# Optimization experiments

Hardware: AMD Instinct MI355X
Metric: run time of the kernel (lower is better)

The kernel has to match this reference:

```python
import jax, jax.numpy as jnp
import numpy as np


def setup_inputs() -> dict:
    key = jax.random.key(0)
    k1, k2, k3 = jax.random.split(key, 3)
    B, C, H, W = 16, 256, 48, 48
    INTER = C // 2
    x = jax.random.normal(k1, (B, C, H, W), dtype=jnp.float32)
    # nn.init.normal_(weight, std=0.01); 1x1 conv kernels stored as (out, in)
    theta_w = 0.01 * jax.random.normal(k2, (INTER, C), dtype=jnp.float32)
    phi_w = 0.01 * jax.random.normal(k3, (INTER, C), dtype=jnp.float32)
    theta_b = jnp.zeros((INTER,), dtype=jnp.float32)
    phi_b = jnp.zeros((INTER,), dtype=jnp.float32)
    return {"x": x, "theta_w": theta_w, "theta_b": theta_b, "phi_w": phi_w, "phi_b": phi_b}


def reference(x, theta_w, theta_b, phi_w, phi_b):
    b, c, h, w = x.shape
    inter = theta_w.shape[0]
    n = h * w
    # 1x1 conv == channel-wise linear projection
    theta_x = jnp.einsum('bchw,kc->bkhw', x, theta_w) + theta_b[None, :, None, None]
    phi_x = jnp.einsum('bchw,kc->bkhw', x, phi_w) + phi_b[None, :, None, None]
    q = theta_x.reshape(b, inter, n)   # [b, k, n]
    kmat = phi_x.reshape(b, inter, n)  # [b, k, n]
    g = x.reshape(b, c, n)             # [b, c, n]
    # f = theta^T @ phi : [b, n, n], scaled then softmaxed over last dim
    f = jnp.einsum('bkn,bkm->bnm', q, kmat) / jnp.sqrt(jnp.asarray(inter, x.dtype))
    f = jax.nn.softmax(f, axis=-1)
    # y = f @ g^T : [b, c, n]
    y = jnp.einsum('bnm,bcm->bcn', f, g)
    return y.reshape(b, c, h, w)
```

## Files before the change

### kernel.cpp

```cpp
#include <hip/hip_runtime.h>
#include <hip/hip_bf16.h>

#define B_SZ 16
#define C_IN 256
#define N_SP 2304
#define K_INT 128
#define NTILE 36
#define MT 32
#define MITER 72

typedef __attribute__((ext_vector_type(8))) short short8;
typedef __attribute__((ext_vector_type(4))) float f32x4;

__device__ inline unsigned pk_bf16(float a, float b) {
  float2 f; f.x = a; f.y = b;
  __hip_bfloat162 h = __float22bfloat162_rn(f);
  unsigned u;
  __builtin_memcpy(&u, &h, sizeof(u));
  return u;
}

__global__ __launch_bounds__(256) void proj_kernel(
    const float* __restrict__ x,
    const float* __restrict__ theta_w, const float* __restrict__ theta_b,
    const float* __restrict__ phi_w,   const float* __restrict__ phi_b,
    short* __restrict__ Qt, short* __restrict__ Kt, short* __restrict__ Gbf)
{
  __shared__ short Xl[64][264];

  const int b  = blockIdx.x / NTILE;
  const int n0 = (blockIdx.x % NTILE) * 64;
  const int t  = threadIdx.x;

  {
    const float* xrow = x + ((size_t)b * C_IN + t) * N_SP + n0;
    unsigned tp[32];
#pragma unroll
    for (int i = 0; i < 16; ++i) {
      float4 v = ((const float4*)xrow)[i];
      tp[2*i]   = pk_bf16(v.x, v.y);
      tp[2*i+1] = pk_bf16(v.z, v.w);
    }
    uint4* grow = (uint4*)(Gbf + ((size_t)b * C_IN + t) * N_SP + n0);
#pragma unroll
    for (int i = 0; i < 8; ++i) {
      uint4 u; u.x = tp[4*i]; u.y = tp[4*i+1]; u.z = tp[4*i+2]; u.w = tp[4*i+3];
      grow[i] = u;
    }
#pragma unroll
    for (int j = 0; j < 32; ++j) {
      Xl[2*j][t]   = (short)tp[j];
      Xl[2*j+1][t] = (short)(tp[j] >> 16);
    }
  }
  __syncthreads();

  const int wave = t >> 6, lane = t & 63;
  const int col = lane & 15, quad = lane >> 4;

  f32x4 acc[2][2][4];
#pragma unroll
  for (int p = 0; p < 2; ++p)
#pragma unroll
    for (int kr = 0; kr < 2; ++kr)
#pragma unroll
      for (int j = 0; j < 4; ++j) {
        acc[p][kr][j][0] = 0.f; acc[p][kr][j][1] = 0.f;
        acc[p][kr][j][2] = 0.f; acc[p][kr][j][3] = 0.f;
      }

#pragma unroll
  for (int cs = 0; cs < 8; ++cs) {
    const int c0 = cs * 32;
    short8 afr[2][2];
#pragma unroll
    for (int p = 0; p < 2; ++p) {
      const float* W = p ? phi_w : theta_w;
#pragma unroll
      for (int kr = 0; kr < 2; ++kr) {
        const int k = wave * 32 + kr * 16 + col;
        const float* wp = W + (size_t)k * C_IN + c0 + quad * 8;
        float4 w0 = ((const float4*)wp)[0];
        float4 w1 = ((const float4*)wp)[1];
        unsigned u[4];
        u[0] = pk_bf16(w0.x, w0.y); u[1] = pk_bf16(w0.z, w0.w);
        u[2] = pk_bf16(w1.x, w1.y); u[3] = pk_bf16(w1.z, w1.w);
        short8 a;
        __builtin_memcpy(&a, u, sizeof(a));
        afr[p][kr] = a;
      }
    }
#pragma unroll
    for (int j = 0; j < 4; ++j) {
      short8 bfr = *(const short8*)&Xl[j * 16 + col][c0 + quad * 8];
#pragma unroll
      for (int p = 0; p < 2; ++p)
#pragma unroll
        for (int kr = 0; kr < 2; ++kr)
          acc[p][kr][j] = __builtin_amdgcn_mfma_f32_16x16x32_bf16(
              afr[p][kr], bfr, acc[p][kr][j], 0, 0, 0);
    }
  }

#pragma unroll
  for (int p = 0; p < 2; ++p) {
    const float* bias = p ? phi_b : theta_b;
    short* dst = p ? Kt : Qt;
#pragma unroll
    for (int kr = 0; kr < 2; ++kr) {
      const int k0 = wave * 32 + kr * 16 + quad * 4;
      float4 bv = *(const float4*)(bias + k0);
#pragma unroll
      for (int j = 0; j < 4; ++j) {
        const int n = n0 + j * 16 + col;
        f32x4 v = acc[p][kr][j];
        uint2 sv;
        sv.x = pk_bf16(v[0] + bv.x, v[1] + bv.y);
        sv.y = pk_bf16(v[2] + bv.z, v[3] + bv.w);
        *(uint2*)(dst + ((size_t)b * N_SP + n) * K_INT + k0) = sv;
      }
    }
  }
}

__global__ __launch_bounds__(256) void attn_kernel(
    const short* __restrict__ Qt, const short* __restrict__ Kt,
    const short* __restrict__ Gbf, float* __restrict__ out)
{
  __shared__ __align__(16) char smem[49152];

  const int b   = blockIdx.x / NTILE;
  const int qn0 = (blockIdx.x % NTILE) * 64;
  const int t = threadIdx.x;
  const int wave = t >> 6, lane = t & 63;
  const int col = lane & 15, quad = lane >> 4;

  const short* Ktb = Kt  + (size_t)b * N_SP * K_INT;
  const short* Gb  = Gbf + (size_t)b * C_IN * N_SP;

  short8 qf[4];
  {
    const short* qb = Qt + ((size_t)b * N_SP + qn0 + wave * 16 + col) * K_INT + quad * 8;
#pragma unroll
    for (int kk = 0; kk < 4; ++kk) qf[kk] = *(const short8*)(qb + kk * 32);
  }

  f32x4 yacc[16];
#pragma unroll
  for (int i = 0; i < 16; ++i) {
    yacc[i][0] = 0.f; yacc[i][1] = 0.f; yacc[i][2] = 0.f; yacc[i][3] = 0.f;
  }
  f32x4 lacc;
  lacc[0] = 0.f; lacc[1] = 0.f; lacc[2] = 0.f; lacc[3] = 0.f;

  short8 ones;
#pragma unroll
  for (int j = 0; j < 8; ++j) ones[j] = (short)0x3F80;

  const float SC2 = 0.12754859f;

  const int KW = (t >> 4) * 256 + ((((t & 15) ^ ((t >> 4) & 7))) << 4);
  const int GW = 8192 + (t >> 2) * 64 + ((((t & 3) ^ ((t >> 3) & 3))) << 4);
  int KR[4];
#pragma unroll
  for (int kk = 0; kk < 4; ++kk)
    KR[kk] = col * 256 + ((((kk << 2) + quad) ^ (col & 7)) << 4);
  const int GR = 8192 + col * 64 + ((quad ^ ((col >> 1) & 3)) << 4);

  const int koff = (t >> 4) * K_INT + (t & 15) * 8;
  const int goff = (t >> 2) * N_SP + (t & 3) * 8;

  short8 pre[6];
  pre[0] = *(const short8*)(Ktb + koff);
  pre[1] = *(const short8*)(Ktb + 2048 + koff);
#pragma unroll
  for (int i = 0; i < 4; ++i) pre[2 + i] = *(const short8*)(Gb + i * 64 * N_SP + goff);
  *(short8*)(smem + KW) = pre[0];
  *(short8*)(smem + KW + 4096) = pre[1];
#pragma unroll
  for (int i = 0; i < 4; ++i) *(short8*)(smem + GW + i * 4096) = pre[2 + i];
  pre[0] = *(const short8*)(Ktb + 4096 + koff);
  pre[1] = *(const short8*)(Ktb + 6144 + koff);
#pragma unroll
  for (int i = 0; i < 4; ++i) pre[2 + i] = *(const short8*)(Gb + 32 + i * 64 * N_SP + goff);
  const short* kptr = Ktb + 8192 + koff;
  const short* gptr = Gb + 64 + goff;
  __syncthreads();

#define SUBITER(MTV, RD, WR)                                                   \
  {                                                                            \
    if ((MTV) + 1 < MITER) {                                                   \
      *(short8*)(smem + KW + (WR)) = pre[0];                                   \
      *(short8*)(smem + KW + (WR) + 4096) = pre[1];                            \
      _Pragma("unroll")                                                        \
      for (int i = 0; i < 4; ++i)                                              \
        *(short8*)(smem + GW + (WR) + i * 4096) = pre[2 + i];                  \
      if ((MTV) + 2 < MITER) {                                                 \
        pre[0] = *(const short8*)(kptr);                                       \
        pre[1] = *(const short8*)(kptr + 2048);                                \
        _Pragma("unroll")                                                      \
        for (int i = 0; i < 4; ++i)                                            \
          pre[2 + i] = *(const short8*)(gptr + i * 64 * N_SP);                 \
        kptr += 4096; gptr += 32;                                              \
      }                                                                        \
    }                                                                          \
    f32x4 s0, s1;                                                              \
    s0[0] = 0.f; s0[1] = 0.f; s0[2] = 0.f; s0[3] = 0.f;                        \
    s1[0] = 0.f; s1[1] = 0.f; s1[2] = 0.f; s1[3] = 0.f;                        \
    _Pragma("unroll")                                                          \
    for (int kk = 0; kk < 4; ++kk) {                                           \
      short8 a0 = *(const short8*)(smem + KR[kk] + (RD));                      \
      s0 = __builtin_amdgcn_mfma_f32_16x16x32_bf16(a0, qf[kk], s0, 0, 0, 0);   \
      short8 a1 = *(const short8*)(smem + KR[kk] + (RD) + 4096);               \
      s1 = __builtin_amdgcn_mfma_f32_16x16x32_bf16(a1, qf[kk], s1, 0, 0, 0);   \
    }                                                                          \
    unsigned u0 = pk_bf16(exp2f(s0[0] * SC2), exp2f(s0[1] * SC2));             \
    unsigned u1 = pk_bf16(exp2f(s0[2] * SC2), exp2f(s0[3] * SC2));             \
    unsigned u2 = pk_bf16(exp2f(s1[0] * SC2), exp2f(s1[1] * SC2));             \
    unsigned u3 = pk_bf16(exp2f(s1[2] * SC2), exp2f(s1[3] * SC2));             \
    asm("v_permlane32_swap_b32 %0, %1" : "+v"(u0), "+v"(u2));                  \
    asm("v_permlane32_swap_b32 %0, %1" : "+v"(u1), "+v"(u3));                  \
    asm("v_permlane16_swap_b32 %0, %1" : "+v"(u0), "+v"(u2));                  \
    asm("v_permlane16_swap_b32 %0, %1" : "+v"(u1), "+v"(u3));                  \
    unsigned uu[4] = {u0, u1, u2, u3};                                         \
    short8 pa; __builtin_memcpy(&pa, uu, 16);                                  \
    _Pragma("unroll")                                                          \
    for (int ct = 0; ct < 16; ++ct) {                                          \
      short8 gb = *(const short8*)(smem + GR + (RD) + ct * 1024);              \
      yacc[ct] = __builtin_amdgcn_mfma_f32_16x16x32_bf16(pa, gb, yacc[ct], 0, 0, 0); \
    }                                                                          \
    lacc = __builtin_amdgcn_mfma_f32_16x16x32_bf16(pa, ones, lacc, 0, 0, 0);   \
    __syncthreads();                                                           \
  }

  for (int mt2 = 0; mt2 < MITER / 2; ++mt2) {
    SUBITER(2 * mt2, 0, 24576)
    SUBITER(2 * mt2 + 1, 24576, 0)
  }
#undef SUBITER

  float inv[4];
#pragma unroll
  for (int r = 0; r < 4; ++r) inv[r] = 1.0f / lacc[r];
  const int nb = qn0 + wave * 16 + quad * 4;
#pragma unroll
  for (int ct = 0; ct < 16; ++ct) {
    int c = ct * 16 + col;
    float4 v;
    v.x = yacc[ct][0] * inv[0]; v.y = yacc[ct][1] * inv[1];
    v.z = yacc[ct][2] * inv[2]; v.w = yacc[ct][3] * inv[3];
    *(float4*)(out + ((size_t)b * C_IN + c) * N_SP + nb) = v;
  }
}

extern "C" void kernel_launch(void* const* d_in, const int* in_sizes, int n_in,
                              void* d_out, int out_size, void* d_ws, size_t ws_size,
                              hipStream_t stream) {
  const float* x  = (const float*)d_in[0];
  const float* tw = (const float*)d_in[1];
  const float* tb = (const float*)d_in[2];
  const float* pw = (const float*)d_in[3];
  const float* pb = (const float*)d_in[4];
  float* out = (float*)d_out;

  short* Qt  = (short*)d_ws;
  short* Kt  = Qt + (size_t)B_SZ * N_SP * K_INT;
  short* Gbf = Kt + (size_t)B_SZ * N_SP * K_INT;

  proj_kernel<<<B_SZ * NTILE, 256, 0, stream>>>(x, tw, tb, pw, pb, Qt, Kt, Gbf);
  attn_kernel<<<B_SZ * NTILE, 256, 0, stream>>>(Qt, Kt, Gbf, out);
}
```

Before: 268.9 us.

## Share P tiles across waves via LDS and split channels per wave in attention

```diff
diff --git a/kernel.cpp b/kernel.cpp
--- a/kernel.cpp
+++ b/kernel.cpp
@@ -12,6 +12,8 @@
 typedef __attribute__((ext_vector_type(8))) short short8;
 typedef __attribute__((ext_vector_type(4))) float f32x4;
 
+__device__ __align__(16) short g_Wbf[2 * K_INT * C_IN];
+
 __device__ inline unsigned pk_bf16(float a, float b) {
   float2 f; f.x = a; f.y = b;
   __hip_bfloat162 h = __float22bfloat162_rn(f);
@@ -20,10 +22,21 @@
   return u;
 }
 
+__global__ __launch_bounds__(256) void wcvt_kernel(
+    const float* __restrict__ tw, const float* __restrict__ pw)
+{
+  const int i = (blockIdx.x * 256 + threadIdx.x) * 4;
+  float4 a = *(const float4*)(tw + i);
+  float4 p = *(const float4*)(pw + i);
+  uint2 ua; ua.x = pk_bf16(a.x, a.y); ua.y = pk_bf16(a.z, a.w);
+  uint2 up; up.x = pk_bf16(p.x, p.y); up.y = pk_bf16(p.z, p.w);
+  *(uint2*)(g_Wbf + i) = ua;
+  *(uint2*)(g_Wbf + 32768 + i) = up;
+}
+
 __global__ __launch_bounds__(256) void proj_kernel(
     const float* __restrict__ x,
-    const float* __restrict__ theta_w, const float* __restrict__ theta_b,
-    const float* __restrict__ phi_w,   const float* __restrict__ phi_b,
+    const float* __restrict__ theta_b, const float* __restrict__ phi_b,
     short* __restrict__ Qt, short* __restrict__ Kt, short* __restrict__ Gbf)
 {
   __shared__ short Xl[64][264];
@@ -74,22 +87,12 @@
     const int c0 = cs * 32;
     short8 afr[2][2];
 #pragma unroll
-    for (int p = 0; p < 2; ++p) {
-      const float* W = p ? phi_w : theta_w;
+    for (int p = 0; p < 2; ++p)
 #pragma unroll
       for (int kr = 0; kr < 2; ++kr) {
         const int k = wave * 32 + kr * 16 + col;
-        const float* wp = W + (size_t)k * C_IN + c0 + quad * 8;
-        float4 w0 = ((const float4*)wp)[0];
-        float4 w1 = ((const float4*)wp)[1];
-        unsigned u[4];
-        u[0] = pk_bf16(w0.x, w0.y); u[1] = pk_bf16(w0.z, w0.w);
-        u[2] = pk_bf16(w1.x, w1.y); u[3] = pk_bf16(w1.z, w1.w);
-        short8 a;
-        __builtin_memcpy(&a, u, sizeof(a));
-        afr[p][kr] = a;
+        afr[p][kr] = *(const short8*)(g_Wbf + p * 32768 + k * C_IN + c0 + quad * 8);
       }
-    }
 #pragma unroll
     for (int j = 0; j < 4; ++j) {
       short8 bfr = *(const short8*)&Xl[j * 16 + col][c0 + quad * 8];
@@ -127,7 +130,8 @@
     const short* __restrict__ Qt, const short* __restrict__ Kt,
     const short* __restrict__ Gbf, float* __restrict__ out)
 {
-  __shared__ __align__(16) char smem[49152];
+  __shared__ __align__(16) char smem[53504];
+  float* l_lds = (float*)(smem + 53248);
 
   const int b   = blockIdx.x / NTILE;
   const int qn0 = (blockIdx.x % NTILE) * 64;
@@ -145,11 +149,14 @@
     for (int kk = 0; kk < 4; ++kk) qf[kk] = *(const short8*)(qb + kk * 32);
   }
 
-  f32x4 yacc[16];
-#pragma unroll
-  for (int i = 0; i < 16; ++i) {
-    yacc[i][0] = 0.f; yacc[i][1] = 0.f; yacc[i][2] = 0.f; yacc[i][3] = 0.f;
-  }
+  f32x4 yacc[4][4];
+#pragma unroll
+  for (int i = 0; i < 4; ++i)
+#pragma unroll
+    for (int j = 0; j < 4; ++j) {
+      yacc[i][j][0] = 0.f; yacc[i][j][1] = 0.f;
+      yacc[i][j][2] = 0.f; yacc[i][j][3] = 0.f;
+    }
   f32x4 lacc;
   lacc[0] = 0.f; lacc[1] = 0.f; lacc[2] = 0.f; lacc[3] = 0.f;
 
@@ -159,13 +166,15 @@
 
   const float SC2 = 0.12754859f;
 
-  const int KW = (t >> 4) * 256 + ((((t & 15) ^ ((t >> 4) & 7))) << 4);
+  const int KW = (t >> 4) * 256 + (((t & 15) ^ ((((t >> 5) & 7)) << 1)) << 4);
   const int GW = 8192 + (t >> 2) * 64 + ((((t & 3) ^ ((t >> 3) & 3))) << 4);
   int KR[4];
 #pragma unroll
   for (int kk = 0; kk < 4; ++kk)
-    KR[kk] = col * 256 + ((((kk << 2) + quad) ^ (col & 7)) << 4);
-  const int GR = 8192 + col * 64 + ((quad ^ ((col >> 1) & 3)) << 4);
+    KR[kk] = col * 256 + ((((kk << 2) + quad) ^ ((((col >> 1) & 7)) << 1)) << 4);
+  const int GR = 8192 + wave * 4096 + col * 64 + ((quad ^ ((col >> 1) & 3)) << 4);
+  const int PW = 49152 + wave * 1024 + col * 64 + quad * 16;
+  const int PR = 49152 + col * 64 + quad * 16;
 
   const int koff = (t >> 4) * K_INT + (t & 15) * 8;
   const int goff = (t >> 2) * N_SP + (t & 3) * 8;
@@ -224,13 +233,22 @@
     asm("v_permlane16_swap_b32 %0, %1" : "+v"(u1), "+v"(u3));                  \
     unsigned uu[4] = {u0, u1, u2, u3};                                         \
     short8 pa; __builtin_memcpy(&pa, uu, 16);                                  \
+    lacc = __builtin_amdgcn_mfma_f32_16x16x32_bf16(pa, ones, lacc, 0, 0, 0);   \
+    *(short8*)(smem + PW) = pa;                                                \
+    __syncthreads();                               \
+    short8 paq[4];                                                             \
     _Pragma("unroll")                                                          \
-    for (int ct = 0; ct < 16; ++ct) {                                          \
+    for (int qt = 0; qt < 4; ++qt)                                             \
+      paq[qt] = *(const short8*)(smem + PR + qt * 1024);                       \
+    _Pragma("unroll")                                                          \
+    for (int ct = 0; ct < 4; ++ct) {                                           \
       short8 gb = *(const short8*)(smem + GR + (RD) + ct * 1024);              \
-      yacc[ct] = __builtin_amdgcn_mfma_f32_16x16x32_bf16(pa, gb, yacc[ct], 0, 0, 0); \
+      _Pragma("unroll")                                                        \
+      for (int qt = 0; qt < 4; ++qt)                                           \
+        yacc[qt][ct] = __builtin_amdgcn_mfma_f32_16x16x32_bf16(                \
+            paq[qt], gb, yacc[qt][ct], 0, 0, 0);                               \
     }                                                                          \
-    lacc = __builtin_amdgcn_mfma_f32_16x16x32_bf16(pa, ones, lacc, 0, 0, 0);   \
-    __syncthreads();                                                           \
+    __syncthreads();          \
   }
 
   for (int mt2 = 0; mt2 < MITER / 2; ++mt2) {
@@ -239,17 +257,26 @@
   }
 #undef SUBITER
 
-  float inv[4];
-#pragma unroll
-  for (int r = 0; r < 4; ++r) inv[r] = 1.0f / lacc[r];
-  const int nb = qn0 + wave * 16 + quad * 4;
-#pragma unroll
-  for (int ct = 0; ct < 16; ++ct) {
-    int c = ct * 16 + col;
-    float4 v;
-    v.x = yacc[ct][0] * inv[0]; v.y = yacc[ct][1] * inv[1];
-    v.z = yacc[ct][2] * inv[2]; v.w = yacc[ct][3] * inv[3];
-    *(float4*)(out + ((size_t)b * C_IN + c) * N_SP + nb) = v;
+  if (col == 0) {
+#pragma unroll
+    for (int r = 0; r < 4; ++r) l_lds[wave * 16 + quad * 4 + r] = lacc[r];
+  }
+  __syncthreads();
+
+#pragma unroll
+  for (int qt = 0; qt < 4; ++qt) {
+    float4 lq = *(const float4*)&l_lds[qt * 16 + quad * 4];
+    float4 iv;
+    iv.x = 1.0f / lq.x; iv.y = 1.0f / lq.y; iv.z = 1.0f / lq.z; iv.w = 1.0f / lq.w;
+    const int nb = qn0 + qt * 16 + quad * 4;
+#pragma unroll
+    for (int ct = 0; ct < 4; ++ct) {
+      const int c = wave * 64 + ct * 16 + col;
+      f32x4 v = yacc[qt][ct];
+      float4 o;
+      o.x = v[0] * iv.x; o.y = v[1] * iv.y; o.z = v[2] * iv.z; o.w = v[3] * iv.w;
+      *(float4*)(out + ((size_t)b * C_IN + c) * N_SP + nb) = o;
+    }
   }
 }
 
@@ -267,6 +294,7 @@
   short* Kt  = Qt + (size_t)B_SZ * N_SP * K_INT;
   short* Gbf = Kt + (size_t)B_SZ * N_SP * K_INT;
 
-  proj_kernel<<<B_SZ * NTILE, 256, 0, stream>>>(x, tw, tb, pw, pb, Qt, Kt, Gbf);
+  wcvt_kernel<<<32, 256, 0, stream>>>(tw, pw);
+  proj_kernel<<<B_SZ * NTILE, 256, 0, stream>>>(x, tb, pb, Qt, Kt, Gbf);
   attn_kernel<<<B_SZ * NTILE, 256, 0, stream>>>(Qt, Kt, Gbf, out);
 }
```

Result: faster. 257.3 us (-4.3%).
